# Kernel optimization log

Measured on AMD Instinct MI355X. Metric: run time of the kernel, lower is better.

Reference implementation:

```python
import jax, jax.numpy as jnp
import numpy as np

NUM_QUANTS = 256
RES_CH = 120
SKIP_CH = 240
K = 2
NUM_BLOCKS = 16
CYCLE = 8
DILATIONS = [2 ** (i % CYCLE) for i in range(NUM_BLOCKS)]


def causal_conv1d(x, w, b, dilation=1):
    # x: [B, Cin, T], w: [Cout, Cin, K], left-pad for causality
    pad = (w.shape[-1] - 1) * dilation
    y = jax.lax.conv_general_dilated(
        x, w, window_strides=(1,), padding=[(pad, 0)],
        rhs_dilation=(dilation,), dimension_numbers=('NCH', 'OIH', 'NCH'))
    return y + b[None, :, None]


def setup_inputs() -> dict:
    key = jax.random.key(0)
    ks = jax.random.split(key, 16)
    B, T = 8, 16384
    s = 0.1
    inp = {
        'waveforms': jax.random.normal(ks[0], (B, T), jnp.float32),
        'W_in': jax.random.normal(ks[1], (RES_CH, 1, 1), jnp.float32) * s,
        'b_in': jnp.zeros((RES_CH,), jnp.float32),
        'Wf': jax.random.normal(ks[2], (NUM_BLOCKS, RES_CH, RES_CH, K), jnp.float32) * s,
        'bf': jnp.zeros((NUM_BLOCKS, RES_CH), jnp.float32),
        'Wg': jax.random.normal(ks[3], (NUM_BLOCKS, RES_CH, RES_CH, K), jnp.float32) * s,
        'bg': jnp.zeros((NUM_BLOCKS, RES_CH), jnp.float32),
        'Wres': jax.random.normal(ks[4], (NUM_BLOCKS, RES_CH, RES_CH, 1), jnp.float32) * s,
        'bres': jnp.zeros((NUM_BLOCKS, RES_CH), jnp.float32),
        'Wskip': jax.random.normal(ks[5], (NUM_BLOCKS, SKIP_CH, RES_CH, 1), jnp.float32) * s,
        'bskip': jnp.zeros((NUM_BLOCKS, SKIP_CH), jnp.float32),
        'W1': jax.random.normal(ks[6], (NUM_QUANTS, SKIP_CH, 1), jnp.float32) * s,
        'b1': jnp.zeros((NUM_QUANTS,), jnp.float32),
        'W2': jax.random.normal(ks[7], (NUM_QUANTS, NUM_QUANTS, 1), jnp.float32) * s,
        'b2': jnp.zeros((NUM_QUANTS,), jnp.float32),
    }
    return inp


def reference(waveforms, W_in, b_in, Wf, bf, Wg, bg, Wres, bres, Wskip, bskip, W1, b1, W2, b2):
    # input 1x1 conv: [B, T] -> [B, RES_CH, T]
    x = causal_conv1d(waveforms[:, None, :], W_in, b_in)
    skip_sum = jnp.zeros((x.shape[0], SKIP_CH, x.shape[2]), x.dtype)
    for i in range(NUM_BLOCKS):
        d = DILATIONS[i]
        f = jnp.tanh(causal_conv1d(x, Wf[i], bf[i], d))
        g = jax.nn.sigmoid(causal_conv1d(x, Wg[i], bg[i], d))
        z = f * g  # gated activation
        skip_sum = skip_sum + causal_conv1d(z, Wskip[i], bskip[i])
        x = x + causal_conv1d(z, Wres[i], bres[i])
    h = jax.nn.relu(skip_sum)
    h = jax.nn.relu(causal_conv1d(h, W1, b1))
    logits = causal_conv1d(h, W2, b2)  # [B, NUM_QUANTS, T]
    return logits
```

## Files before the change

### kernel.cpp

```cpp
#include <hip/hip_runtime.h>
#include <cstddef>

#define TT 16384
#define NBATCH 8
#define CH 128
#define RES 120
#define SKIPC 240
#define NQ 256
#define NT 64
#define KZ 2048

typedef __attribute__((ext_vector_type(8))) short bf8;
typedef __attribute__((ext_vector_type(4))) short s4;
typedef __attribute__((ext_vector_type(4))) float f32x4;

__device__ __forceinline__ short f2bf(float f) {
  unsigned u = __builtin_bit_cast(unsigned, f);
  u += 0x7fffu + ((u >> 16) & 1u);
  return (short)(u >> 16);
}
__device__ __forceinline__ float bf2f(short s) {
  unsigned u = ((unsigned)(unsigned short)s) << 16;
  return __builtin_bit_cast(float, u);
}

__global__ void k_pack(const float* __restrict__ Wf, const float* __restrict__ Wg,
                       const float* __restrict__ Wres, const float* __restrict__ Wskip,
                       const float* __restrict__ W1, const float* __restrict__ W2,
                       const float* __restrict__ bf, const float* __restrict__ bg,
                       const float* __restrict__ bres, const float* __restrict__ bskip,
                       short* __restrict__ Afg, short* __restrict__ Ars,
                       short* __restrict__ W1p, short* __restrict__ W2p,
                       float* __restrict__ biasp,
                       short* __restrict__ Wskp, float* __restrict__ bsum, int do2) {
  const int NAFG = 16 * 256 * 256;
  const int NARS = 16 * 384 * 128;
  const int NW = 256 * 256;
  const int NBIA = 16 * (128 * 3 + 256);
  const int NWSK = 256 * 2048;
  const int total = NAFG + NARS + 2 * NW + NBIA + NWSK + 256;
  for (int idx = blockIdx.x * blockDim.x + threadIdx.x; idx < total;
       idx += gridDim.x * blockDim.x) {
    if (idx < NAFG) {
      int i = idx >> 16, rem = idx & 65535, m = rem >> 8, k = rem & 255;
      int tap = k >> 7, ci = k & 127;
      float v = 0.f;
      if (ci < 120) {
        if (m < 120) v = Wf[((i * 120 + m) * 120 + ci) * 2 + tap];
        else if (m >= 128 && m < 248) v = Wg[((i * 120 + (m - 128)) * 120 + ci) * 2 + tap];
      }
      Afg[idx] = f2bf(v);
    } else if (idx < NAFG + NARS) {
      int j = idx - NAFG;
      int i = j / 49152, rem = j % 49152, m = rem >> 7, k = rem & 127;
      float v = 0.f;
      if (k < 120) {
        if (m < 120) v = Wres[(i * 120 + m) * 120 + k];
        else if (m >= 128 && m < 368) v = Wskip[(i * 240 + (m - 128)) * 120 + k];
      }
      Ars[j] = f2bf(v);
    } else if (idx < NAFG + NARS + NW) {
      int j = idx - NAFG - NARS, q = j >> 8, k = j & 255;
      W1p[j] = f2bf(k < 240 ? W1[q * 240 + k] : 0.f);
    } else if (idx < NAFG + NARS + 2 * NW) {
      int j = idx - NAFG - NARS - NW;
      W2p[j] = f2bf(W2[j]);
    } else if (idx < NAFG + NARS + 2 * NW + NBIA) {
      int j = idx - NAFG - NARS - 2 * NW;
      float v = 0.f;
      if (j < 2048) { int i = j >> 7, c = j & 127; if (c < 120) v = bf[i * 120 + c]; }
      else if (j < 4096) { int jj = j - 2048; int i = jj >> 7, c = jj & 127; if (c < 120) v = bg[i * 120 + c]; }
      else if (j < 6144) { int jj = j - 4096; int i = jj >> 7, c = jj & 127; if (c < 120) v = bres[i * 120 + c]; }
      else { int jj = j - 6144; int i = jj >> 8, c = jj & 255; if (c < 240) v = bskip[i * 240 + c]; }
      biasp[j] = v;
    } else if (idx < NAFG + NARS + 2 * NW + NBIA + NWSK) {
      if (do2) {
        int j = idx - NAFG - NARS - 2 * NW - NBIA;
        int m = j >> 11, k = j & 2047;
        int layer = k >> 7, ci = k & 127;
        float v = 0.f;
        if (m < 240 && ci < 120) v = Wskip[((size_t)layer * 240 + m) * 120 + ci];
        Wskp[j] = f2bf(v);
      }
    } else {
      if (do2) {
        int m = idx - (NAFG + NARS + 2 * NW + NBIA + NWSK);
        float v = 0.f;
        if (m < 240)
          for (int l = 0; l < 16; l++) v += bskip[l * 240 + m];
        bsum[m] = v;
      }
    }
  }
}

__global__ void k_input(const float* __restrict__ wave, const float* __restrict__ win,
                        const float* __restrict__ bin, short* __restrict__ x0) {
  int idx = blockIdx.x * blockDim.x + threadIdx.x;
  if (idx >= NBATCH * TT) return;
  float wv = wave[idx];
  short* row = x0 + (size_t)idx * CH;
  for (int c = 0; c < CH; c += 4) {
    s4 v;
#pragma unroll
    for (int j = 0; j < 4; j++)
      v[j] = (c + j < 120) ? f2bf(win[c + j] * wv + bin[c + j]) : (short)0;
    *(s4*)(row + c) = v;
  }
}

__global__ __launch_bounds__(256) void k_res2(
    const short* __restrict__ xin, short* __restrict__ xout,
    short* __restrict__ zg,
    const short* __restrict__ Afg, const short* __restrict__ Ars,
    const float* __restrict__ biasp, int layer, int dil, int b_off) {
  __shared__ short zT[NT][136];
  const int bl = blockIdx.y;
  const int b = b_off + bl;
  const int t0 = blockIdx.x * NT;
  const int tid = threadIdx.x;
  const int lane = tid & 63, w = tid >> 6;
  const int l15 = lane & 15, l4 = lane >> 4;
  const size_t xbase = (size_t)b * TT * CH;

  f32x4 fa[2][4], ga[2][4];
#pragma unroll
  for (int i = 0; i < 2; i++)
#pragma unroll
    for (int j = 0; j < 4; j++) { fa[i][j] = (f32x4)0.f; ga[i][j] = (f32x4)0.f; }

  const short* pBd[4];
  const short* pBc[4];
  bool vld[4];
#pragma unroll
  for (int nt = 0; nt < 4; nt++) {
    int t = t0 + nt * 16 + l15;
    int ts = t - dil;
    vld[nt] = (ts >= 0);
    pBd[nt] = xin + xbase + (size_t)(vld[nt] ? ts : 0) * CH + l4 * 8;
    pBc[nt] = xin + xbase + (size_t)t * CH + l4 * 8;
  }
  const short* pAf[2];
  const short* pAg[2];
#pragma unroll
  for (int mt = 0; mt < 2; mt++) {
    pAf[mt] = Afg + (size_t)(w * 32 + mt * 16 + l15) * 256 + l4 * 8;
    pAg[mt] = Afg + (size_t)(128 + w * 32 + mt * 16 + l15) * 256 + l4 * 8;
  }
  const bf8 zv = (bf8)(short)0;
#pragma unroll
  for (int kk = 0; kk < 8; kk++) {
    const int k = kk * 32;
    bf8 Bv[4];
#pragma unroll
    for (int nt = 0; nt < 4; nt++) {
      if (kk < 4) {
        bf8 v = *(const bf8*)(pBd[nt] + k);
        Bv[nt] = vld[nt] ? v : zv;
      } else {
        Bv[nt] = *(const bf8*)(pBc[nt] + (k - 128));
      }
    }
#pragma unroll
    for (int mt = 0; mt < 2; mt++) {
      bf8 Av = *(const bf8*)(pAf[mt] + k);
      bf8 Gv = *(const bf8*)(pAg[mt] + k);
#pragma unroll
      for (int nt = 0; nt < 4; nt++) {
        fa[mt][nt] = __builtin_amdgcn_mfma_f32_16x16x32_bf16(Av, Bv[nt], fa[mt][nt], 0, 0, 0);
        ga[mt][nt] = __builtin_amdgcn_mfma_f32_16x16x32_bf16(Gv, Bv[nt], ga[mt][nt], 0, 0, 0);
      }
    }
  }

  const float* bf_ = biasp + (size_t)layer * 128;
  const float* bg_ = biasp + 2048 + (size_t)layer * 128;
#pragma unroll
  for (int mt = 0; mt < 2; mt++) {
    int mb = w * 32 + mt * 16 + l4 * 4;
#pragma unroll
    for (int nt = 0; nt < 4; nt++) {
      s4 zp;
#pragma unroll
      for (int r = 0; r < 4; r++) {
        float f = fa[mt][nt][r] + bf_[mb + r];
        float g = ga[mt][nt][r] + bg_[mb + r];
        float th = 1.f - 2.f / (__expf(2.f * f) + 1.f);
        float sg = 1.f / (1.f + __expf(-g));
        zp[r] = f2bf(th * sg);
      }
      *(s4*)&zT[nt * 16 + l15][mb] = zp;
    }
  }
  __syncthreads();

  for (int u = tid; u < NT * 16; u += 256) {
    int t = u >> 4, c8 = u & 15;
    bf8 v = *(const bf8*)&zT[t][c8 * 8];
    *(bf8*)(zg + ((size_t)(bl * TT + t0 + t) * 16 + layer) * 128 + c8 * 8) = v;
  }

  f32x4 acc[2][4];
#pragma unroll
  for (int i = 0; i < 2; i++)
#pragma unroll
    for (int j = 0; j < 4; j++) acc[i][j] = (f32x4)0.f;
  const short* pA[2];
#pragma unroll
  for (int mt = 0; mt < 2; mt++)
    pA[mt] = Ars + (size_t)(w * 32 + mt * 16 + l15) * 128 + l4 * 8;
#pragma unroll
  for (int kk = 0; kk < 4; kk++) {
    const int k = kk * 32;
    bf8 Bv[4];
#pragma unroll
    for (int nt = 0; nt < 4; nt++) Bv[nt] = *(const bf8*)&zT[nt * 16 + l15][k + l4 * 8];
#pragma unroll
    for (int mt = 0; mt < 2; mt++) {
      bf8 Av = *(const bf8*)(pA[mt] + k);
#pragma unroll
      for (int nt = 0; nt < 4; nt++)
        acc[mt][nt] = __builtin_amdgcn_mfma_f32_16x16x32_bf16(Av, Bv[nt], acc[mt][nt], 0, 0, 0);
    }
  }

  const float* br_ = biasp + 4096 + (size_t)layer * 128;
#pragma unroll
  for (int mt = 0; mt < 2; mt++) {
    int m = w * 32 + mt * 16 + l4 * 4;
#pragma unroll
    for (int nt = 0; nt < 4; nt++) {
      int t = t0 + nt * 16 + l15;
      s4 xv = *(const s4*)(xin + xbase + (size_t)t * CH + m);
      s4 ov;
#pragma unroll
      for (int r = 0; r < 4; r++)
        ov[r] = f2bf(bf2f(xv[r]) + acc[mt][nt][r] + br_[m + r]);
      *(s4*)(xout + xbase + (size_t)t * CH + m) = ov;
    }
  }
}

__global__ __launch_bounds__(256) void k_head2(
    const short* __restrict__ zg, const short* __restrict__ Wskp,
    const float* __restrict__ bsum,
    const short* __restrict__ W1p, const float* __restrict__ b1,
    const short* __restrict__ W2p, const float* __restrict__ b2,
    float* __restrict__ out, int b_off) {
  __shared__ short hT[NT][264];
  const int bl = blockIdx.y;
  const int b = b_off + bl;
  const int t0 = blockIdx.x * NT;
  const int tid = threadIdx.x;
  const int lane = tid & 63, w = tid >> 6;
  const int l15 = lane & 15, l4 = lane >> 4;

  f32x4 acc[4][4];
#pragma unroll
  for (int i = 0; i < 4; i++)
#pragma unroll
    for (int j = 0; j < 4; j++) acc[i][j] = (f32x4)0.f;

  const short* pB[4];
#pragma unroll
  for (int nt = 0; nt < 4; nt++)
    pB[nt] = zg + (size_t)(bl * TT + t0 + nt * 16 + l15) * KZ + l4 * 8;
  const short* pA[4];
#pragma unroll
  for (int mt = 0; mt < 4; mt++)
    pA[mt] = Wskp + (size_t)(w * 64 + mt * 16 + l15) * KZ + l4 * 8;
  for (int kk = 0; kk < KZ / 32; kk++) {
    const int k = kk * 32;
    bf8 Bv[4];
#pragma unroll
    for (int nt = 0; nt < 4; nt++) Bv[nt] = *(const bf8*)(pB[nt] + k);
#pragma unroll
    for (int mt = 0; mt < 4; mt++) {
      bf8 Av = *(const bf8*)(pA[mt] + k);
#pragma unroll
      for (int nt = 0; nt < 4; nt++)
        acc[mt][nt] = __builtin_amdgcn_mfma_f32_16x16x32_bf16(Av, Bv[nt], acc[mt][nt], 0, 0, 0);
    }
  }
#pragma unroll
  for (int mt = 0; mt < 4; mt++) {
    int mb = w * 64 + mt * 16 + l4 * 4;
#pragma unroll
    for (int nt = 0; nt < 4; nt++) {
      s4 hp;
#pragma unroll
      for (int r = 0; r < 4; r++)
        hp[r] = f2bf(fmaxf(acc[mt][nt][r] + bsum[mb + r], 0.f));
      *(s4*)&hT[nt * 16 + l15][mb] = hp;
    }
  }
  __syncthreads();

#pragma unroll
  for (int i = 0; i < 4; i++)
#pragma unroll
    for (int j = 0; j < 4; j++) acc[i][j] = (f32x4)0.f;
#pragma unroll
  for (int kk = 0; kk < 8; kk++) {
    const int k = kk * 32;
    bf8 Bv[4];
#pragma unroll
    for (int nt = 0; nt < 4; nt++) Bv[nt] = *(const bf8*)&hT[nt * 16 + l15][k + l4 * 8];
#pragma unroll
    for (int mt = 0; mt < 4; mt++) {
      bf8 Av = *(const bf8*)(W1p + (size_t)(w * 64 + mt * 16 + l15) * 256 + k + l4 * 8);
#pragma unroll
      for (int nt = 0; nt < 4; nt++)
        acc[mt][nt] = __builtin_amdgcn_mfma_f32_16x16x32_bf16(Av, Bv[nt], acc[mt][nt], 0, 0, 0);
    }
  }
  __syncthreads();
#pragma unroll
  for (int mt = 0; mt < 4; mt++) {
    int mb = w * 64 + mt * 16 + l4 * 4;
#pragma unroll
    for (int nt = 0; nt < 4; nt++) {
      s4 hp;
#pragma unroll
      for (int r = 0; r < 4; r++)
        hp[r] = f2bf(fmaxf(acc[mt][nt][r] + b1[mb + r], 0.f));
      *(s4*)&hT[nt * 16 + l15][mb] = hp;
    }
  }
  __syncthreads();

#pragma unroll
  for (int i = 0; i < 4; i++)
#pragma unroll
    for (int j = 0; j < 4; j++) acc[i][j] = (f32x4)0.f;
#pragma unroll
  for (int kk = 0; kk < 8; kk++) {
    const int k = kk * 32;
    bf8 Bv[4];
#pragma unroll
    for (int nt = 0; nt < 4; nt++) Bv[nt] = *(const bf8*)&hT[nt * 16 + l15][k + l4 * 8];
#pragma unroll
    for (int mt = 0; mt < 4; mt++) {
      bf8 Av = *(const bf8*)(W2p + (size_t)(w * 64 + mt * 16 + l15) * 256 + k + l4 * 8);
#pragma unroll
      for (int nt = 0; nt < 4; nt++)
        acc[mt][nt] = __builtin_amdgcn_mfma_f32_16x16x32_bf16(Av, Bv[nt], acc[mt][nt], 0, 0, 0);
    }
  }
#pragma unroll
  for (int mt = 0; mt < 4; mt++) {
    int q = w * 64 + mt * 16 + l4 * 4;
#pragma unroll
    for (int nt = 0; nt < 4; nt++) {
      int t = t0 + nt * 16 + l15;
#pragma unroll
      for (int r = 0; r < 4; r++)
        out[((size_t)b * NQ + q + r) * TT + t] = acc[mt][nt][r] + b2[q + r];
    }
  }
}

__global__ __launch_bounds__(256) void k_res_mfma(
    const short* __restrict__ xin, short* __restrict__ xout,
    float* __restrict__ skip,
    const short* __restrict__ Afg, const short* __restrict__ Ars,
    const float* __restrict__ biasp, int layer, int dil, int first) {
  __shared__ short zT[NT][136];
  const int b = blockIdx.y;
  const int t0 = blockIdx.x * NT;
  const int tid = threadIdx.x;
  const int lane = tid & 63, w = tid >> 6;
  const int l15 = lane & 15, l4 = lane >> 4;
  const size_t xbase = (size_t)b * TT * CH;

  f32x4 fa[2][4], ga[2][4];
#pragma unroll
  for (int i = 0; i < 2; i++)
#pragma unroll
    for (int j = 0; j < 4; j++) { fa[i][j] = (f32x4)0.f; ga[i][j] = (f32x4)0.f; }

  const short* pBd[4];
  const short* pBc[4];
  bool vld[4];
#pragma unroll
  for (int nt = 0; nt < 4; nt++) {
    int t = t0 + nt * 16 + l15;
    int ts = t - dil;
    vld[nt] = (ts >= 0);
    pBd[nt] = xin + xbase + (size_t)(vld[nt] ? ts : 0) * CH + l4 * 8;
    pBc[nt] = xin + xbase + (size_t)t * CH + l4 * 8;
  }
  const short* pAf[2];
  const short* pAg[2];
#pragma unroll
  for (int mt = 0; mt < 2; mt++) {
    pAf[mt] = Afg + (size_t)(w * 32 + mt * 16 + l15) * 256 + l4 * 8;
    pAg[mt] = Afg + (size_t)(128 + w * 32 + mt * 16 + l15) * 256 + l4 * 8;
  }
  const bf8 zv = (bf8)(short)0;
#pragma unroll
  for (int kk = 0; kk < 8; kk++) {
    const int k = kk * 32;
    bf8 Bv[4];
#pragma unroll
    for (int nt = 0; nt < 4; nt++) {
      if (kk < 4) {
        bf8 v = *(const bf8*)(pBd[nt] + k);
        Bv[nt] = vld[nt] ? v : zv;
      } else {
        Bv[nt] = *(const bf8*)(pBc[nt] + (k - 128));
      }
    }
#pragma unroll
    for (int mt = 0; mt < 2; mt++) {
      bf8 Av = *(const bf8*)(pAf[mt] + k);
      bf8 Gv = *(const bf8*)(pAg[mt] + k);
#pragma unroll
      for (int nt = 0; nt < 4; nt++) {
        fa[mt][nt] = __builtin_amdgcn_mfma_f32_16x16x32_bf16(Av, Bv[nt], fa[mt][nt], 0, 0, 0);
        ga[mt][nt] = __builtin_amdgcn_mfma_f32_16x16x32_bf16(Gv, Bv[nt], ga[mt][nt], 0, 0, 0);
      }
    }
  }

  const float* bf_ = biasp + (size_t)layer * 128;
  const float* bg_ = biasp + 2048 + (size_t)layer * 128;
#pragma unroll
  for (int mt = 0; mt < 2; mt++) {
    int mb = w * 32 + mt * 16 + l4 * 4;
#pragma unroll
    for (int nt = 0; nt < 4; nt++) {
      s4 zp;
#pragma unroll
      for (int r = 0; r < 4; r++) {
        float f = fa[mt][nt][r] + bf_[mb + r];
        float g = ga[mt][nt][r] + bg_[mb + r];
        float th = 1.f - 2.f / (__expf(2.f * f) + 1.f);
        float sg = 1.f / (1.f + __expf(-g));
        zp[r] = f2bf(th * sg);
      }
      *(s4*)&zT[nt * 16 + l15][mb] = zp;
    }
  }
  __syncthreads();

  f32x4 acc[6][4];
#pragma unroll
  for (int i = 0; i < 6; i++)
#pragma unroll
    for (int j = 0; j < 4; j++) acc[i][j] = (f32x4)0.f;
  const short* pA[6];
#pragma unroll
  for (int mt = 0; mt < 6; mt++)
    pA[mt] = Ars + (size_t)(w * 96 + mt * 16 + l15) * 128 + l4 * 8;
#pragma unroll
  for (int kk = 0; kk < 4; kk++) {
    const int k = kk * 32;
    bf8 Bv[4];
#pragma unroll
    for (int nt = 0; nt < 4; nt++) Bv[nt] = *(const bf8*)&zT[nt * 16 + l15][k + l4 * 8];
#pragma unroll
    for (int mt = 0; mt < 6; mt++) {
      bf8 Av = *(const bf8*)(pA[mt] + k);
#pragma unroll
      for (int nt = 0; nt < 4; nt++)
        acc[mt][nt] = __builtin_amdgcn_mfma_f32_16x16x32_bf16(Av, Bv[nt], acc[mt][nt], 0, 0, 0);
    }
  }

  const float* br_ = biasp + 4096 + (size_t)layer * 128;
  const float* bs_ = biasp + 6144 + (size_t)layer * 256;
#pragma unroll
  for (int mt = 0; mt < 6; mt++) {
    int m = w * 96 + mt * 16 + l4 * 4;
#pragma unroll
    for (int nt = 0; nt < 4; nt++) {
      int t = t0 + nt * 16 + l15;
      if (m < 128) {
        s4 xv = *(const s4*)(xin + xbase + (size_t)t * CH + m);
        s4 ov;
#pragma unroll
        for (int r = 0; r < 4; r++)
          ov[r] = f2bf(bf2f(xv[r]) + acc[mt][nt][r] + br_[m + r]);
        *(s4*)(xout + xbase + (size_t)t * CH + m) = ov;
      } else if (m < 128 + SKIPC) {
        int c = m - 128;
        float* sp = skip + ((size_t)b * NQ + c) * TT + t;
#pragma unroll
        for (int r = 0; r < 4; r++) {
          float v = acc[mt][nt][r] + bs_[c + r];
          if (!first) v += sp[(size_t)r * TT];
          sp[(size_t)r * TT] = v;
        }
      }
    }
  }
}

__global__ __launch_bounds__(256) void k_head_mfma(
    const float* skip, const short* __restrict__ W1p, const float* __restrict__ b1,
    const short* __restrict__ W2p, const float* __restrict__ b2, float* out) {
  __shared__ short hT[NT][264];
  __shared__ short h2T[NT][264];
  const int b = blockIdx.y;
  const int t0 = blockIdx.x * NT;
  const int tid = threadIdx.x;
  const int lane = tid & 63, w = tid >> 6;
  const int l15 = lane & 15, l4 = lane >> 4;

  for (int u = tid; u < 256 * 16; u += 256) {
    int c = u >> 4, tq = u & 15;
    if (c < SKIPC) {
      f32x4 v = *(const f32x4*)(skip + ((size_t)b * NQ + c) * TT + t0 + tq * 4);
#pragma unroll
      for (int j = 0; j < 4; j++) hT[tq * 4 + j][c] = f2bf(fmaxf(v[j], 0.f));
    } else {
#pragma unroll
      for (int j = 0; j < 4; j++) hT[tq * 4 + j][c] = 0;
    }
  }
  __syncthreads();

  f32x4 acc[4][4];
#pragma unroll
  for (int i = 0; i < 4; i++)
#pragma unroll
    for (int j = 0; j < 4; j++) acc[i][j] = (f32x4)0.f;
#pragma unroll
  for (int kk = 0; kk < 8; kk++) {
    const int k = kk * 32;
    bf8 Bv[4];
#pragma unroll
    for (int nt = 0; nt < 4; nt++) Bv[nt] = *(const bf8*)&hT[nt * 16 + l15][k + l4 * 8];
#pragma unroll
    for (int mt = 0; mt < 4; mt++) {
      bf8 Av = *(const bf8*)(W1p + (size_t)(w * 64 + mt * 16 + l15) * 256 + k + l4 * 8);
#pragma unroll
      for (int nt = 0; nt < 4; nt++)
        acc[mt][nt] = __builtin_amdgcn_mfma_f32_16x16x32_bf16(Av, Bv[nt], acc[mt][nt], 0, 0, 0);
    }
  }
#pragma unroll
  for (int mt = 0; mt < 4; mt++) {
    int mb = w * 64 + mt * 16 + l4 * 4;
#pragma unroll
    for (int nt = 0; nt < 4; nt++) {
      s4 hp;
#pragma unroll
      for (int r = 0; r < 4; r++) hp[r] = f2bf(fmaxf(acc[mt][nt][r] + b1[mb + r], 0.f));
      *(s4*)&h2T[nt * 16 + l15][mb] = hp;
    }
  }
  __syncthreads();

#pragma unroll
  for (int i = 0; i < 4; i++)
#pragma unroll
    for (int j = 0; j < 4; j++) acc[i][j] = (f32x4)0.f;
#pragma unroll
  for (int kk = 0; kk < 8; kk++) {
    const int k = kk * 32;
    bf8 Bv[4];
#pragma unroll
    for (int nt = 0; nt < 4; nt++) Bv[nt] = *(const bf8*)&h2T[nt * 16 + l15][k + l4 * 8];
#pragma unroll
    for (int mt = 0; mt < 4; mt++) {
      bf8 Av = *(const bf8*)(W2p + (size_t)(w * 64 + mt * 16 + l15) * 256 + k + l4 * 8);
#pragma unroll
      for (int nt = 0; nt < 4; nt++)
        acc[mt][nt] = __builtin_amdgcn_mfma_f32_16x16x32_bf16(Av, Bv[nt], acc[mt][nt], 0, 0, 0);
    }
  }
#pragma unroll
  for (int mt = 0; mt < 4; mt++) {
    int q = w * 64 + mt * 16 + l4 * 4;
#pragma unroll
    for (int nt = 0; nt < 4; nt++) {
      int t = t0 + nt * 16 + l15;
#pragma unroll
      for (int r = 0; r < 4; r++)
        out[((size_t)b * NQ + q + r) * TT + t] = acc[mt][nt][r] + b2[q + r];
    }
  }
}

extern "C" void kernel_launch(void* const* d_in, const int* in_sizes, int n_in,
                              void* d_out, int out_size, void* d_ws, size_t ws_size,
                              hipStream_t stream) {
  const float* wave  = (const float*)d_in[0];
  const float* W_in  = (const float*)d_in[1];
  const float* b_in  = (const float*)d_in[2];
  const float* Wf    = (const float*)d_in[3];
  const float* bf    = (const float*)d_in[4];
  const float* Wg    = (const float*)d_in[5];
  const float* bg    = (const float*)d_in[6];
  const float* Wres  = (const float*)d_in[7];
  const float* bres  = (const float*)d_in[8];
  const float* Wskip = (const float*)d_in[9];
  const float* bskip = (const float*)d_in[10];
  const float* W1    = (const float*)d_in[11];
  const float* b1    = (const float*)d_in[12];
  const float* W2    = (const float*)d_in[13];
  const float* b2    = (const float*)d_in[14];
  float* out = (float*)d_out;

  char* ws = (char*)d_ws;
  short* xA    = (short*)ws;
  short* xB    = (short*)(ws + 33554432);
  short* Afg   = (short*)(ws + 67108864);
  short* Ars   = (short*)(ws + 69206016);
  short* W1p   = (short*)(ws + 70778880);
  short* W2p   = (short*)(ws + 70909952);
  float* biasp = (float*)(ws + 71041024);
  short* Wskp  = (short*)(ws + 71081984);
  float* bsum  = (float*)(ws + 72130560);
  short* zg    = (short*)(ws + 72131584);
  const size_t BASE = 72131584ull;
  const size_t ZPB  = (size_t)TT * KZ * 2;

  int nbg = 0;
  if      (ws_size >= BASE + 8 * ZPB) nbg = 8;
  else if (ws_size >= BASE + 4 * ZPB) nbg = 4;
  else if (ws_size >= BASE + 2 * ZPB) nbg = 2;
  else if (ws_size >= BASE + 1 * ZPB) nbg = 1;
  const int do2 = (ws_size >= BASE) ? 1 : 0;

  k_pack<<<1024, 256, 0, stream>>>(Wf, Wg, Wres, Wskip, W1, W2, bf, bg, bres, bskip,
                                   Afg, Ars, W1p, W2p, biasp, Wskp, bsum, do2);
  k_input<<<(NBATCH * TT) / 256, 256, 0, stream>>>(wave, W_in, b_in, xA);

  static const int dils[16] = {1, 2, 4, 8, 16, 32, 64, 128,
                               1, 2, 4, 8, 16, 32, 64, 128};
  if (nbg > 0) {
    for (int g = 0; g < NBATCH; g += nbg) {
      const short* xi = xA;
      short* xo = xB;
      for (int i = 0; i < 16; i++) {
        k_res2<<<dim3(TT / NT, nbg), 256, 0, stream>>>(
            xi, xo, zg, Afg + (size_t)i * 65536, Ars + (size_t)i * 49152,
            biasp, i, dils[i], g);
        short* tmp = (short*)xi; xi = xo; xo = tmp;
      }
      k_head2<<<dim3(TT / NT, nbg), 256, 0, stream>>>(zg, Wskp, bsum, W1p, b1,
                                                      W2p, b2, out, g);
    }
  } else {
    const short* xi = xA;
    short* xo = xB;
    for (int i = 0; i < 16; i++) {
      k_res_mfma<<<dim3(TT / NT, NBATCH), 256, 0, stream>>>(
          xi, xo, out, Afg + (size_t)i * 65536, Ars + (size_t)i * 49152,
          biasp, i, dils[i], i == 0 ? 1 : 0);
      short* tmp = (short*)xi; xi = xo; xo = tmp;
    }
    k_head_mfma<<<dim3(TT / NT, NBATCH), 256, 0, stream>>>(out, W1p, b1, W2p, b2, out);
  }
}
```

Baseline: 2.278 ms.

## Shrink time tiles to 32 with 512-thread blocks and prefetch skip GEMM loads

The batched-z path (k_res2, k_head2) now processes 32 time steps per block using 8 waves of 512 threads, each wave handling 16 output channels. The grid doubles and each wave holds fewer accumulators, which is meant to raise occupancy and parallelism. The long K=2048 skip GEMM in k_head2 gets a register double-buffered prefetch of the next A/B fragments, and the zg and output stores become nontemporal. The trade-off is that weight fragments are reused across fewer time columns, so more weight traffic is issued per output. The k_pack flag now depends on nbg rather than do2.

```diff
diff --git a/kernel.cpp b/kernel.cpp
--- a/kernel.cpp
+++ b/kernel.cpp
@@ -7,7 +7,8 @@
 #define RES 120
 #define SKIPC 240
 #define NQ 256
-#define NT 64
+#define NT2 32
+#define NTF 64
 #define KZ 2048
 
 typedef __attribute__((ext_vector_type(8))) short bf8;
@@ -109,15 +110,240 @@
   }
 }
 
-__global__ __launch_bounds__(256) void k_res2(
+__global__ __launch_bounds__(512) void k_res2(
     const short* __restrict__ xin, short* __restrict__ xout,
     short* __restrict__ zg,
     const short* __restrict__ Afg, const short* __restrict__ Ars,
     const float* __restrict__ biasp, int layer, int dil, int b_off) {
-  __shared__ short zT[NT][136];
+  __shared__ short zT[NT2][136];
   const int bl = blockIdx.y;
   const int b = b_off + bl;
-  const int t0 = blockIdx.x * NT;
+  const int t0 = blockIdx.x * NT2;
+  const int tid = threadIdx.x;
+  const int lane = tid & 63, w = tid >> 6;
+  const int l15 = lane & 15, l4 = lane >> 4;
+  const size_t xbase = (size_t)b * TT * CH;
+
+  f32x4 fa[2], ga[2];
+  fa[0] = (f32x4)0.f; fa[1] = (f32x4)0.f; ga[0] = (f32x4)0.f; ga[1] = (f32x4)0.f;
+
+  const short* pBd[2];
+  const short* pBc[2];
+  bool vld[2];
+#pragma unroll
+  for (int nt = 0; nt < 2; nt++) {
+    int t = t0 + nt * 16 + l15;
+    int ts = t - dil;
+    vld[nt] = (ts >= 0);
+    pBd[nt] = xin + xbase + (size_t)(vld[nt] ? ts : 0) * CH + l4 * 8;
+    pBc[nt] = xin + xbase + (size_t)t * CH + l4 * 8;
+  }
+  const short* pAf = Afg + (size_t)(w * 16 + l15) * 256 + l4 * 8;
+  const short* pAg = Afg + (size_t)(128 + w * 16 + l15) * 256 + l4 * 8;
+  const bf8 zv = (bf8)(short)0;
+#pragma unroll
+  for (int kk = 0; kk < 8; kk++) {
+    const int k = kk * 32;
+    bf8 Bv[2];
+#pragma unroll
+    for (int nt = 0; nt < 2; nt++) {
+      if (kk < 4) {
+        bf8 v = *(const bf8*)(pBd[nt] + k);
+        Bv[nt] = vld[nt] ? v : zv;
+      } else {
+        Bv[nt] = *(const bf8*)(pBc[nt] + (k - 128));
+      }
+    }
+    bf8 Av = *(const bf8*)(pAf + k);
+    bf8 Gv = *(const bf8*)(pAg + k);
+#pragma unroll
+    for (int nt = 0; nt < 2; nt++) {
+      fa[nt] = __builtin_amdgcn_mfma_f32_16x16x32_bf16(Av, Bv[nt], fa[nt], 0, 0, 0);
+      ga[nt] = __builtin_amdgcn_mfma_f32_16x16x32_bf16(Gv, Bv[nt], ga[nt], 0, 0, 0);
+    }
+  }
+
+  const float* bf_ = biasp + (size_t)layer * 128;
+  const float* bg_ = biasp + 2048 + (size_t)layer * 128;
+  const int mb = w * 16 + l4 * 4;
+#pragma unroll
+  for (int nt = 0; nt < 2; nt++) {
+    s4 zp;
+#pragma unroll
+    for (int r = 0; r < 4; r++) {
+      float f = fa[nt][r] + bf_[mb + r];
+      float g = ga[nt][r] + bg_[mb + r];
+      float th = 1.f - 2.f / (__expf(2.f * f) + 1.f);
+      float sg = 1.f / (1.f + __expf(-g));
+      zp[r] = f2bf(th * sg);
+    }
+    *(s4*)&zT[nt * 16 + l15][mb] = zp;
+  }
+  __syncthreads();
+
+  {
+    const int u = tid;
+    const int t = u >> 4, c8 = u & 15;
+    bf8 v = *(const bf8*)&zT[t][c8 * 8];
+    __builtin_nontemporal_store(
+        v, (bf8*)(zg + ((size_t)(bl * TT + t0 + t) * 16 + layer) * 128 + c8 * 8));
+  }
+
+  f32x4 acc[2];
+  acc[0] = (f32x4)0.f; acc[1] = (f32x4)0.f;
+  const short* pA = Ars + (size_t)(w * 16 + l15) * 128 + l4 * 8;
+#pragma unroll
+  for (int kk = 0; kk < 4; kk++) {
+    const int k = kk * 32;
+    bf8 Bv[2];
+#pragma unroll
+    for (int nt = 0; nt < 2; nt++) Bv[nt] = *(const bf8*)&zT[nt * 16 + l15][k + l4 * 8];
+    bf8 Av = *(const bf8*)(pA + k);
+#pragma unroll
+    for (int nt = 0; nt < 2; nt++)
+      acc[nt] = __builtin_amdgcn_mfma_f32_16x16x32_bf16(Av, Bv[nt], acc[nt], 0, 0, 0);
+  }
+
+  const float* br_ = biasp + 4096 + (size_t)layer * 128;
+  const int m = w * 16 + l4 * 4;
+#pragma unroll
+  for (int nt = 0; nt < 2; nt++) {
+    int t = t0 + nt * 16 + l15;
+    s4 xv = *(const s4*)(xin + xbase + (size_t)t * CH + m);
+    s4 ov;
+#pragma unroll
+    for (int r = 0; r < 4; r++)
+      ov[r] = f2bf(bf2f(xv[r]) + acc[nt][r] + br_[m + r]);
+    *(s4*)(xout + xbase + (size_t)t * CH + m) = ov;
+  }
+}
+
+__global__ __launch_bounds__(512) void k_head2(
+    const short* __restrict__ zg, const short* __restrict__ Wskp,
+    const float* __restrict__ bsum,
+    const short* __restrict__ W1p, const float* __restrict__ b1,
+    const short* __restrict__ W2p, const float* __restrict__ b2,
+    float* __restrict__ out, int b_off) {
+  __shared__ short hT[NT2][264];
+  const int bl = blockIdx.y;
+  const int b = b_off + bl;
+  const int t0 = blockIdx.x * NT2;
+  const int tid = threadIdx.x;
+  const int lane = tid & 63, w = tid >> 6;
+  const int l15 = lane & 15, l4 = lane >> 4;
+
+  f32x4 acc[2][2];
+#pragma unroll
+  for (int i = 0; i < 2; i++)
+#pragma unroll
+    for (int j = 0; j < 2; j++) acc[i][j] = (f32x4)0.f;
+
+  const short* pB0 = zg + (size_t)(bl * TT + t0 + l15) * KZ + l4 * 8;
+  const short* pB1 = zg + (size_t)(bl * TT + t0 + 16 + l15) * KZ + l4 * 8;
+  const short* pA0 = Wskp + (size_t)(w * 32 + l15) * KZ + l4 * 8;
+  const short* pA1 = Wskp + (size_t)(w * 32 + 16 + l15) * KZ + l4 * 8;
+  bf8 B0 = *(const bf8*)pB0, B1 = *(const bf8*)pB1;
+  bf8 A0 = *(const bf8*)pA0, A1 = *(const bf8*)pA1;
+  for (int kk = 0; kk < 64; kk++) {
+    const int ko = ((kk + 1) & 63) * 32;
+    bf8 nB0 = *(const bf8*)(pB0 + ko);
+    bf8 nB1 = *(const bf8*)(pB1 + ko);
+    bf8 nA0 = *(const bf8*)(pA0 + ko);
+    bf8 nA1 = *(const bf8*)(pA1 + ko);
+    acc[0][0] = __builtin_amdgcn_mfma_f32_16x16x32_bf16(A0, B0, acc[0][0], 0, 0, 0);
+    acc[0][1] = __builtin_amdgcn_mfma_f32_16x16x32_bf16(A0, B1, acc[0][1], 0, 0, 0);
+    acc[1][0] = __builtin_amdgcn_mfma_f32_16x16x32_bf16(A1, B0, acc[1][0], 0, 0, 0);
+    acc[1][1] = __builtin_amdgcn_mfma_f32_16x16x32_bf16(A1, B1, acc[1][1], 0, 0, 0);
+    B0 = nB0; B1 = nB1; A0 = nA0; A1 = nA1;
+  }
+#pragma unroll
+  for (int mt = 0; mt < 2; mt++) {
+    int mb = w * 32 + mt * 16 + l4 * 4;
+#pragma unroll
+    for (int nt = 0; nt < 2; nt++) {
+      s4 hp;
+#pragma unroll
+      for (int r = 0; r < 4; r++)
+        hp[r] = f2bf(fmaxf(acc[mt][nt][r] + bsum[mb + r], 0.f));
+      *(s4*)&hT[nt * 16 + l15][mb] = hp;
+    }
+  }
+  __syncthreads();
+
+#pragma unroll
+  for (int i = 0; i < 2; i++)
+#pragma unroll
+    for (int j = 0; j < 2; j++) acc[i][j] = (f32x4)0.f;
+#pragma unroll
+  for (int kk = 0; kk < 8; kk++) {
+    const int k = kk * 32;
+    bf8 Bv[2];
+#pragma unroll
+    for (int nt = 0; nt < 2; nt++) Bv[nt] = *(const bf8*)&hT[nt * 16 + l15][k + l4 * 8];
+#pragma unroll
+    for (int mt = 0; mt < 2; mt++) {
+      bf8 Av = *(const bf8*)(W1p + (size_t)(w * 32 + mt * 16 + l15) * 256 + k + l4 * 8);
+#pragma unroll
+      for (int nt = 0; nt < 2; nt++)
+        acc[mt][nt] = __builtin_amdgcn_mfma_f32_16x16x32_bf16(Av, Bv[nt], acc[mt][nt], 0, 0, 0);
+    }
+  }
+  __syncthreads();
+#pragma unroll
+  for (int mt = 0; mt < 2; mt++) {
+    int mb = w * 32 + mt * 16 + l4 * 4;
+#pragma unroll
+    for (int nt = 0; nt < 2; nt++) {
+      s4 hp;
+#pragma unroll
+      for (int r = 0; r < 4; r++)
+        hp[r] = f2bf(fmaxf(acc[mt][nt][r] + b1[mb + r], 0.f));
+      *(s4*)&hT[nt * 16 + l15][mb] = hp;
+    }
+  }
+  __syncthreads();
+
+#pragma unroll
+  for (int i = 0; i < 2; i++)
+#pragma unroll
+    for (int j = 0; j < 2; j++) acc[i][j] = (f32x4)0.f;
+#pragma unroll
+  for (int kk = 0; kk < 8; kk++) {
+    const int k = kk * 32;
+    bf8 Bv[2];
+#pragma unroll
+    for (int nt = 0; nt < 2; nt++) Bv[nt] = *(const bf8*)&hT[nt * 16 + l15][k + l4 * 8];
+#pragma unroll
+    for (int mt = 0; mt < 2; mt++) {
+      bf8 Av = *(const bf8*)(W2p + (size_t)(w * 32 + mt * 16 + l15) * 256 + k + l4 * 8);
+#pragma unroll
+      for (int nt = 0; nt < 2; nt++)
+        acc[mt][nt] = __builtin_amdgcn_mfma_f32_16x16x32_bf16(Av, Bv[nt], acc[mt][nt], 0, 0, 0);
+    }
+  }
+#pragma unroll
+  for (int mt = 0; mt < 2; mt++) {
+    int q = w * 32 + mt * 16 + l4 * 4;
+#pragma unroll
+    for (int nt = 0; nt < 2; nt++) {
+      int t = t0 + nt * 16 + l15;
+#pragma unroll
+      for (int r = 0; r < 4; r++) {
+        float v = acc[mt][nt][r] + b2[q + r];
+        __builtin_nontemporal_store(v, out + ((size_t)b * NQ + q + r) * TT + t);
+      }
+    }
+  }
+}
+
+__global__ __launch_bounds__(256) void k_res_mfma(
+    const short* __restrict__ xin, short* __restrict__ xout,
+    float* __restrict__ skip,
+    const short* __restrict__ Afg, const short* __restrict__ Ars,
+    const float* __restrict__ biasp, int layer, int dil, int first) {
+  __shared__ short zT[NTF][136];
+  const int b = blockIdx.y;
+  const int t0 = blockIdx.x * NTF;
   const int tid = threadIdx.x;
   const int lane = tid & 63, w = tid >> 6;
   const int l15 = lane & 15, l4 = lane >> 4;
@@ -194,256 +420,6 @@
   }
   __syncthreads();
 
-  for (int u = tid; u < NT * 16; u += 256) {
-    int t = u >> 4, c8 = u & 15;
-    bf8 v = *(const bf8*)&zT[t][c8 * 8];
-    *(bf8*)(zg + ((size_t)(bl * TT + t0 + t) * 16 + layer) * 128 + c8 * 8) = v;
-  }
-
-  f32x4 acc[2][4];
-#pragma unroll
-  for (int i = 0; i < 2; i++)
-#pragma unroll
-    for (int j = 0; j < 4; j++) acc[i][j] = (f32x4)0.f;
-  const short* pA[2];
-#pragma unroll
-  for (int mt = 0; mt < 2; mt++)
-    pA[mt] = Ars + (size_t)(w * 32 + mt * 16 + l15) * 128 + l4 * 8;
-#pragma unroll
-  for (int kk = 0; kk < 4; kk++) {
-    const int k = kk * 32;
-    bf8 Bv[4];
-#pragma unroll
-    for (int nt = 0; nt < 4; nt++) Bv[nt] = *(const bf8*)&zT[nt * 16 + l15][k + l4 * 8];
-#pragma unroll
-    for (int mt = 0; mt < 2; mt++) {
-      bf8 Av = *(const bf8*)(pA[mt] + k);
-#pragma unroll
-      for (int nt = 0; nt < 4; nt++)
-        acc[mt][nt] = __builtin_amdgcn_mfma_f32_16x16x32_bf16(Av, Bv[nt], acc[mt][nt], 0, 0, 0);
-    }
-  }
-
-  const float* br_ = biasp + 4096 + (size_t)layer * 128;
-#pragma unroll
-  for (int mt = 0; mt < 2; mt++) {
-    int m = w * 32 + mt * 16 + l4 * 4;
-#pragma unroll
-    for (int nt = 0; nt < 4; nt++) {
-      int t = t0 + nt * 16 + l15;
-      s4 xv = *(const s4*)(xin + xbase + (size_t)t * CH + m);
-      s4 ov;
-#pragma unroll
-      for (int r = 0; r < 4; r++)
-        ov[r] = f2bf(bf2f(xv[r]) + acc[mt][nt][r] + br_[m + r]);
-      *(s4*)(xout + xbase + (size_t)t * CH + m) = ov;
-    }
-  }
-}
-
-__global__ __launch_bounds__(256) void k_head2(
-    const short* __restrict__ zg, const short* __restrict__ Wskp,
-    const float* __restrict__ bsum,
-    const short* __restrict__ W1p, const float* __restrict__ b1,
-    const short* __restrict__ W2p, const float* __restrict__ b2,
-    float* __restrict__ out, int b_off) {
-  __shared__ short hT[NT][264];
-  const int bl = blockIdx.y;
-  const int b = b_off + bl;
-  const int t0 = blockIdx.x * NT;
-  const int tid = threadIdx.x;
-  const int lane = tid & 63, w = tid >> 6;
-  const int l15 = lane & 15, l4 = lane >> 4;
-
-  f32x4 acc[4][4];
-#pragma unroll
-  for (int i = 0; i < 4; i++)
-#pragma unroll
-    for (int j = 0; j < 4; j++) acc[i][j] = (f32x4)0.f;
-
-  const short* pB[4];
-#pragma unroll
-  for (int nt = 0; nt < 4; nt++)
-    pB[nt] = zg + (size_t)(bl * TT + t0 + nt * 16 + l15) * KZ + l4 * 8;
-  const short* pA[4];
-#pragma unroll
-  for (int mt = 0; mt < 4; mt++)
-    pA[mt] = Wskp + (size_t)(w * 64 + mt * 16 + l15) * KZ + l4 * 8;
-  for (int kk = 0; kk < KZ / 32; kk++) {
-    const int k = kk * 32;
-    bf8 Bv[4];
-#pragma unroll
-    for (int nt = 0; nt < 4; nt++) Bv[nt] = *(const bf8*)(pB[nt] + k);
-#pragma unroll
-    for (int mt = 0; mt < 4; mt++) {
-      bf8 Av = *(const bf8*)(pA[mt] + k);
-#pragma unroll
-      for (int nt = 0; nt < 4; nt++)
-        acc[mt][nt] = __builtin_amdgcn_mfma_f32_16x16x32_bf16(Av, Bv[nt], acc[mt][nt], 0, 0, 0);
-    }
-  }
-#pragma unroll
-  for (int mt = 0; mt < 4; mt++) {
-    int mb = w * 64 + mt * 16 + l4 * 4;
-#pragma unroll
-    for (int nt = 0; nt < 4; nt++) {
-      s4 hp;
-#pragma unroll
-      for (int r = 0; r < 4; r++)
-        hp[r] = f2bf(fmaxf(acc[mt][nt][r] + bsum[mb + r], 0.f));
-      *(s4*)&hT[nt * 16 + l15][mb] = hp;
-    }
-  }
-  __syncthreads();
-
-#pragma unroll
-  for (int i = 0; i < 4; i++)
-#pragma unroll
-    for (int j = 0; j < 4; j++) acc[i][j] = (f32x4)0.f;
-#pragma unroll
-  for (int kk = 0; kk < 8; kk++) {
-    const int k = kk * 32;
-    bf8 Bv[4];
-#pragma unroll
-    for (int nt = 0; nt < 4; nt++) Bv[nt] = *(const bf8*)&hT[nt * 16 + l15][k + l4 * 8];
-#pragma unroll
-    for (int mt = 0; mt < 4; mt++) {
-      bf8 Av = *(const bf8*)(W1p + (size_t)(w * 64 + mt * 16 + l15) * 256 + k + l4 * 8);
-#pragma unroll
-      for (int nt = 0; nt < 4; nt++)
-        acc[mt][nt] = __builtin_amdgcn_mfma_f32_16x16x32_bf16(Av, Bv[nt], acc[mt][nt], 0, 0, 0);
-    }
-  }
-  __syncthreads();
-#pragma unroll
-  for (int mt = 0; mt < 4; mt++) {
-    int mb = w * 64 + mt * 16 + l4 * 4;
-#pragma unroll
-    for (int nt = 0; nt < 4; nt++) {
-      s4 hp;
-#pragma unroll
-      for (int r = 0; r < 4; r++)
-        hp[r] = f2bf(fmaxf(acc[mt][nt][r] + b1[mb + r], 0.f));
-      *(s4*)&hT[nt * 16 + l15][mb] = hp;
-    }
-  }
-  __syncthreads();
-
-#pragma unroll
-  for (int i = 0; i < 4; i++)
-#pragma unroll
-    for (int j = 0; j < 4; j++) acc[i][j] = (f32x4)0.f;
-#pragma unroll
-  for (int kk = 0; kk < 8; kk++) {
-    const int k = kk * 32;
-    bf8 Bv[4];
-#pragma unroll
-    for (int nt = 0; nt < 4; nt++) Bv[nt] = *(const bf8*)&hT[nt * 16 + l15][k + l4 * 8];
-#pragma unroll
-    for (int mt = 0; mt < 4; mt++) {
-      bf8 Av = *(const bf8*)(W2p + (size_t)(w * 64 + mt * 16 + l15) * 256 + k + l4 * 8);
-#pragma unroll
-      for (int nt = 0; nt < 4; nt++)
-        acc[mt][nt] = __builtin_amdgcn_mfma_f32_16x16x32_bf16(Av, Bv[nt], acc[mt][nt], 0, 0, 0);
-    }
-  }
-#pragma unroll
-  for (int mt = 0; mt < 4; mt++) {
-    int q = w * 64 + mt * 16 + l4 * 4;
-#pragma unroll
-    for (int nt = 0; nt < 4; nt++) {
-      int t = t0 + nt * 16 + l15;
-#pragma unroll
-      for (int r = 0; r < 4; r++)
-        out[((size_t)b * NQ + q + r) * TT + t] = acc[mt][nt][r] + b2[q + r];
-    }
-  }
-}
-
-__global__ __launch_bounds__(256) void k_res_mfma(
-    const short* __restrict__ xin, short* __restrict__ xout,
-    float* __restrict__ skip,
-    const short* __restrict__ Afg, const short* __restrict__ Ars,
-    const float* __restrict__ biasp, int layer, int dil, int first) {
-  __shared__ short zT[NT][136];
-  const int b = blockIdx.y;
-  const int t0 = blockIdx.x * NT;
-  const int tid = threadIdx.x;
-  const int lane = tid & 63, w = tid >> 6;
-  const int l15 = lane & 15, l4 = lane >> 4;
-  const size_t xbase = (size_t)b * TT * CH;
-
-  f32x4 fa[2][4], ga[2][4];
-#pragma unroll
-  for (int i = 0; i < 2; i++)
-#pragma unroll
-    for (int j = 0; j < 4; j++) { fa[i][j] = (f32x4)0.f; ga[i][j] = (f32x4)0.f; }
-
-  const short* pBd[4];
-  const short* pBc[4];
-  bool vld[4];
-#pragma unroll
-  for (int nt = 0; nt < 4; nt++) {
-    int t = t0 + nt * 16 + l15;
-    int ts = t - dil;
-    vld[nt] = (ts >= 0);
-    pBd[nt] = xin + xbase + (size_t)(vld[nt] ? ts : 0) * CH + l4 * 8;
-    pBc[nt] = xin + xbase + (size_t)t * CH + l4 * 8;
-  }
-  const short* pAf[2];
-  const short* pAg[2];
-#pragma unroll
-  for (int mt = 0; mt < 2; mt++) {
-    pAf[mt] = Afg + (size_t)(w * 32 + mt * 16 + l15) * 256 + l4 * 8;
-    pAg[mt] = Afg + (size_t)(128 + w * 32 + mt * 16 + l15) * 256 + l4 * 8;
-  }
-  const bf8 zv = (bf8)(short)0;
-#pragma unroll
-  for (int kk = 0; kk < 8; kk++) {
-    const int k = kk * 32;
-    bf8 Bv[4];
-#pragma unroll
-    for (int nt = 0; nt < 4; nt++) {
-      if (kk < 4) {
-        bf8 v = *(const bf8*)(pBd[nt] + k);
-        Bv[nt] = vld[nt] ? v : zv;
-      } else {
-        Bv[nt] = *(const bf8*)(pBc[nt] + (k - 128));
-      }
-    }
-#pragma unroll
-    for (int mt = 0; mt < 2; mt++) {
-      bf8 Av = *(const bf8*)(pAf[mt] + k);
-      bf8 Gv = *(const bf8*)(pAg[mt] + k);
-#pragma unroll
-      for (int nt = 0; nt < 4; nt++) {
-        fa[mt][nt] = __builtin_amdgcn_mfma_f32_16x16x32_bf16(Av, Bv[nt], fa[mt][nt], 0, 0, 0);
-        ga[mt][nt] = __builtin_amdgcn_mfma_f32_16x16x32_bf16(Gv, Bv[nt], ga[mt][nt], 0, 0, 0);
-      }
-    }
-  }
-
-  const float* bf_ = biasp + (size_t)layer * 128;
-  const float* bg_ = biasp + 2048 + (size_t)layer * 128;
-#pragma unroll
-  for (int mt = 0; mt < 2; mt++) {
-    int mb = w * 32 + mt * 16 + l4 * 4;
-#pragma unroll
-    for (int nt = 0; nt < 4; nt++) {
-      s4 zp;
-#pragma unroll
-      for (int r = 0; r < 4; r++) {
-        float f = fa[mt][nt][r] + bf_[mb + r];
-        float g = ga[mt][nt][r] + bg_[mb + r];
-        float th = 1.f - 2.f / (__expf(2.f * f) + 1.f);
-        float sg = 1.f / (1.f + __expf(-g));
-        zp[r] = f2bf(th * sg);
-      }
-      *(s4*)&zT[nt * 16 + l15][mb] = zp;
-    }
-  }
-  __syncthreads();
-
   f32x4 acc[6][4];
 #pragma unroll
   for (int i = 0; i < 6; i++)
@@ -500,10 +476,10 @@
 __global__ __launch_bounds__(256) void k_head_mfma(
     const float* skip, const short* __restrict__ W1p, const float* __restrict__ b1,
     const short* __restrict__ W2p, const float* __restrict__ b2, float* out) {
-  __shared__ short hT[NT][264];
-  __shared__ short h2T[NT][264];
+  __shared__ short hT[NTF][264];
+  __shared__ short h2T[NTF][264];
   const int b = blockIdx.y;
-  const int t0 = blockIdx.x * NT;
+  const int t0 = blockIdx.x * NTF;
   const int tid = threadIdx.x;
   const int lane = tid & 63, w = tid >> 6;
   const int l15 = lane & 15, l4 = lane >> 4;
@@ -626,7 +602,8 @@
   const int do2 = (ws_size >= BASE) ? 1 : 0;
 
   k_pack<<<1024, 256, 0, stream>>>(Wf, Wg, Wres, Wskip, W1, W2, bf, bg, bres, bskip,
-                                   Afg, Ars, W1p, W2p, biasp, Wskp, bsum, do2);
+                                   Afg, Ars, W1p, W2p, biasp, Wskp, bsum,
+                                   nbg > 0 ? 1 : 0);
   k_input<<<(NBATCH * TT) / 256, 256, 0, stream>>>(wave, W_in, b_in, xA);
 
   static const int dils[16] = {1, 2, 4, 8, 16, 32, 64, 128,
@@ -636,23 +613,23 @@
       const short* xi = xA;
       short* xo = xB;
       for (int i = 0; i < 16; i++) {
-        k_res2<<<dim3(TT / NT, nbg), 256, 0, stream>>>(
+        k_res2<<<dim3(TT / NT2, nbg), 512, 0, stream>>>(
             xi, xo, zg, Afg + (size_t)i * 65536, Ars + (size_t)i * 49152,
             biasp, i, dils[i], g);
         short* tmp = (short*)xi; xi = xo; xo = tmp;
       }
-      k_head2<<<dim3(TT / NT, nbg), 256, 0, stream>>>(zg, Wskp, bsum, W1p, b1,
-                                                      W2p, b2, out, g);
+      k_head2<<<dim3(TT / NT2, nbg), 512, 0, stream>>>(zg, Wskp, bsum, W1p, b1,
+                                                       W2p, b2, out, g);
     }
   } else {
     const short* xi = xA;
     short* xo = xB;
     for (int i = 0; i < 16; i++) {
-      k_res_mfma<<<dim3(TT / NT, NBATCH), 256, 0, stream>>>(
+      k_res_mfma<<<dim3(TT / NTF, NBATCH), 256, 0, stream>>>(
           xi, xo, out, Afg + (size_t)i * 65536, Ars + (size_t)i * 49152,
           biasp, i, dils[i], i == 0 ? 1 : 0);
       short* tmp = (short*)xi; xi = xo; xo = tmp;
     }
-    k_head_mfma<<<dim3(TT / NT, NBATCH), 256, 0, stream>>>(out, W1p, b1, W2p, b2, out);
-  }
-}
+    k_head_mfma<<<dim3(TT / NTF, NBATCH), 256, 0, stream>>>(out, W1p, b1, W2p, b2, out);
+  }
+}
```

Measured after the change: 3.574 ms. +56.9%, slower.
